# Kernel optimization log

Measured on AMD Instinct MI355X. Metric: run time of the kernel, lower is better.

Reference implementation:

```python
import jax, jax.numpy as jnp
import numpy as np

B, T, D = 16, 2048, 64


def setup_inputs() -> dict:
    key = jax.random.key(0)
    kq, kk, kv, kb = jax.random.split(key, 4)
    q = jax.random.normal(kq, (B, T, D), dtype=jnp.float32)
    k = jax.random.normal(kk, (B, T, D), dtype=jnp.float32)
    v = jax.random.normal(kv, (B, T, D), dtype=jnp.float32)
    add_attn = jax.random.normal(kb, (B, T, T), dtype=jnp.float32)
    return {"q": q, "k": k, "v": v, "add_attn": add_attn}


def reference(q, k, v, add_attn):
    # scale = 1/sqrt(head_dim), the standard value passed by callers
    scale = 1.0 / jnp.sqrt(jnp.asarray(q.shape[-1], dtype=q.dtype))
    # [B, T, T] attention logits: bmm(q, k^T) * scale + additive bias
    attn = jnp.einsum('btd,bsd->bts', q, k) * scale + add_attn
    # softmax over keys (dim=2); dropout p=0.0 is identity
    attn = jax.nn.softmax(attn, axis=2)
    # [B, T, D] weighted values
    output = jnp.einsum('bts,bsd->btd', attn, v)
    return (output, attn)
```

## Files before the change

### kernel.cpp

```cpp
#include <hip/hip_runtime.h>
#include <stdint.h>

#define NB 16
#define NT 2048
#define ND 64

typedef __attribute__((ext_vector_type(8))) short bf16x8;
typedef __attribute__((ext_vector_type(4))) float f32x4;
typedef __attribute__((ext_vector_type(4))) _Float16 f16x4;

__device__ __forceinline__ unsigned short f2bf(float f) {
    union { float f; unsigned u; } v; v.f = f;
    unsigned r = v.u + 0x7fffu + ((v.u >> 16) & 1u);
    return (unsigned short)(r >> 16);
}
__device__ __forceinline__ unsigned short f2h(float f) {
    union { _Float16 h; unsigned short u; } v; v.h = (_Float16)f; return v.u;
}

__global__ __launch_bounds__(256) void prep_k(const float* __restrict__ Q,
                                              const float* __restrict__ K,
                                              const float* __restrict__ V,
                                              unsigned short* __restrict__ qbf,
                                              unsigned short* __restrict__ kbf,
                                              unsigned short* __restrict__ vt)
{
    const size_t i = (size_t)blockIdx.x * 256 + threadIdx.x;
    const int which = blockIdx.y;
    if (which == 2) {
        float4 v4 = ((const float4*)V)[i];
        const int d4 = (int)(i & 15);
        const int t  = (int)((i >> 4) & (NT - 1));
        const int b  = (int)(i >> 15);
        unsigned short* base = vt + ((size_t)b * ND + d4 * 4) * NT + t;
        base[0]      = f2h(v4.x);
        base[NT]     = f2h(v4.y);
        base[2 * NT] = f2h(v4.z);
        base[3 * NT] = f2h(v4.w);
    } else {
        const float4* src = (which == 0) ? (const float4*)Q : (const float4*)K;
        unsigned short* dst = (which == 0) ? qbf : kbf;
        float4 v4 = src[i];
        union { unsigned short s[4]; unsigned long long ll; } u;
        u.s[0] = f2bf(v4.x); u.s[1] = f2bf(v4.y);
        u.s[2] = f2bf(v4.z); u.s[3] = f2bf(v4.w);
        *(unsigned long long*)(dst + 4 * i) = u.ll;
    }
}

__global__ __launch_bounds__(256, 2)
void attn_onepass(const unsigned short* __restrict__ qbf,
                  const unsigned short* __restrict__ kbf,
                  const unsigned short* __restrict__ vt,
                  const float* __restrict__ Bias,
                  float* __restrict__ Out,
                  float* __restrict__ Attn)
{
    const int b = blockIdx.y, q0 = blockIdx.x * 16;
    const int tid = threadIdx.x, w = tid >> 6, lane = tid & 63;
    const int n = lane & 15, qd = lane >> 4;
    const int kw0 = w * 512;

    __shared__ float s_rs[4][16];
    __shared__ float s_o[4 * 16 * 68];

    const unsigned short* qp = qbf + ((size_t)(b * NT + q0 + n)) * ND + qd * 8;
    const bf16x8 qf0 = *(const bf16x8*)qp;
    const bf16x8 qf1 = *(const bf16x8*)(qp + 32);
    const float* Bb = Bias + ((size_t)b * NT + q0 + n) * NT;
    float* Ab = Attn + ((size_t)b * NT + q0 + n) * NT;
    const unsigned short* vtb = vt + (size_t)b * ND * NT + (size_t)n * NT;

    f16x4 ev[32];
    bf16x8 kb0[6], kb1[6];
    float4 bb[8];
#pragma unroll
    for (int i = 0; i < 6; ++i) {
        const unsigned short* kp = kbf + ((size_t)(b * NT + kw0 + 16 * i + n)) * ND + qd * 8;
        kb0[i] = *(const bf16x8*)kp;
        kb1[i] = *(const bf16x8*)(kp + 32);
    }
#pragma unroll
    for (int i = 0; i < 8; ++i)
        bb[i] = *(const float4*)(Bb + kw0 + 16 * i + qd * 4);
    __builtin_amdgcn_sched_barrier(0);

    float rs = 0.f;
#pragma unroll
    for (int t = 0; t < 32; ++t) {
        const bf16x8 kf0 = kb0[t % 6];
        const bf16x8 kf1 = kb1[t % 6];
        const float4 bs = bb[t & 7];
        f32x4 acc = {0.f, 0.f, 0.f, 0.f};
        acc = __builtin_amdgcn_mfma_f32_16x16x32_bf16(kf0, qf0, acc, 0, 0, 0);
        acc = __builtin_amdgcn_mfma_f32_16x16x32_bf16(kf1, qf1, acc, 0, 0, 0);
        float e0 = __expf(__builtin_fmaf(acc[0], 0.125f, bs.x - 2.0f));
        float e1 = __expf(__builtin_fmaf(acc[1], 0.125f, bs.y - 2.0f));
        float e2 = __expf(__builtin_fmaf(acc[2], 0.125f, bs.z - 2.0f));
        float e3 = __expf(__builtin_fmaf(acc[3], 0.125f, bs.w - 2.0f));
        union { _Float16 h[4]; f16x4 v; } u;
        u.h[0] = (_Float16)e0; u.h[1] = (_Float16)e1;
        u.h[2] = (_Float16)e2; u.h[3] = (_Float16)e3;
        ev[t] = u.v;
        rs += (e0 + e1) + (e2 + e3);
        __builtin_amdgcn_sched_barrier(0);
        if (t + 6 < 32) {
            const unsigned short* kp =
                kbf + ((size_t)(b * NT + kw0 + 16 * (t + 6) + n)) * ND + qd * 8;
            kb0[t % 6] = *(const bf16x8*)kp;
            kb1[t % 6] = *(const bf16x8*)(kp + 32);
        }
        if (t + 8 < 32)
            bb[t & 7] = *(const float4*)(Bb + kw0 + 16 * (t + 8) + qd * 4);
        __builtin_amdgcn_sched_barrier(0);
    }

    f16x4 vr0[4][4], vr1[4][4];
#pragma unroll
    for (int i = 0; i < 4; ++i)
#pragma unroll
        for (int dt = 0; dt < 4; ++dt) {
            const unsigned short* vp = vtb + kw0 + 32 * i + qd * 4 + (size_t)dt * 16 * NT;
            vr0[i][dt] = *(const f16x4*)(const void*)vp;
            vr1[i][dt] = *(const f16x4*)(const void*)(vp + 16);
        }
    __builtin_amdgcn_sched_barrier(0);

    rs += __shfl_xor(rs, 16, 64);
    rs += __shfl_xor(rs, 32, 64);
    if (lane < 16) s_rs[w][lane] = rs;
    __syncthreads();
    const float tot = (s_rs[0][n] + s_rs[1][n]) + (s_rs[2][n] + s_rs[3][n]);
    const float inv = 1.0f / tot;

    f32x4 oacc[4];
#pragma unroll
    for (int dt = 0; dt < 4; ++dt) oacc[dt] = (f32x4){0.f, 0.f, 0.f, 0.f};

#pragma unroll
    for (int tp = 0; tp < 16; ++tp) {
        const int key0 = kw0 + 32 * tp;
        f16x4 va0[4], va1[4];
#pragma unroll
        for (int dt = 0; dt < 4; ++dt) { va0[dt] = vr0[tp & 3][dt]; va1[dt] = vr1[tp & 3][dt]; }
        const f16x4 e0v = ev[2 * tp];
        const f16x4 e1v = ev[2 * tp + 1];
        float4 s0, s1;
        s0.x = (float)e0v[0] * inv; s0.y = (float)e0v[1] * inv;
        s0.z = (float)e0v[2] * inv; s0.w = (float)e0v[3] * inv;
        s1.x = (float)e1v[0] * inv; s1.y = (float)e1v[1] * inv;
        s1.z = (float)e1v[2] * inv; s1.w = (float)e1v[3] * inv;
        *(float4*)(Ab + key0 + qd * 4) = s0;
        *(float4*)(Ab + key0 + 16 + qd * 4) = s1;
#pragma unroll
        for (int dt = 0; dt < 4; ++dt) {
            oacc[dt] = __builtin_amdgcn_mfma_f32_16x16x16f16(va0[dt], e0v, oacc[dt], 0, 0, 0);
            oacc[dt] = __builtin_amdgcn_mfma_f32_16x16x16f16(va1[dt], e1v, oacc[dt], 0, 0, 0);
        }
        __builtin_amdgcn_sched_barrier(0);
        if (tp + 4 < 16) {
#pragma unroll
            for (int dt = 0; dt < 4; ++dt) {
                const unsigned short* vp =
                    vtb + kw0 + 32 * (tp + 4) + qd * 4 + (size_t)dt * 16 * NT;
                vr0[tp & 3][dt] = *(const f16x4*)(const void*)vp;
                vr1[tp & 3][dt] = *(const f16x4*)(const void*)(vp + 16);
            }
        }
        __builtin_amdgcn_sched_barrier(0);
    }

#pragma unroll
    for (int dt = 0; dt < 4; ++dt) {
        float4 t4;
        t4.x = oacc[dt][0] * inv; t4.y = oacc[dt][1] * inv;
        t4.z = oacc[dt][2] * inv; t4.w = oacc[dt][3] * inv;
        *(float4*)&s_o[(w * 16 + n) * 68 + dt * 16 + qd * 4] = t4;
    }
    __syncthreads();
    {
        const int row = tid >> 4, d4 = (tid & 15) * 4;
        float4 o0 = *(const float4*)&s_o[(0 * 16 + row) * 68 + d4];
        float4 o1 = *(const float4*)&s_o[(1 * 16 + row) * 68 + d4];
        float4 o2 = *(const float4*)&s_o[(2 * 16 + row) * 68 + d4];
        float4 o3 = *(const float4*)&s_o[(3 * 16 + row) * 68 + d4];
        float4 o;
        o.x = (o0.x + o1.x) + (o2.x + o3.x);
        o.y = (o0.y + o1.y) + (o2.y + o3.y);
        o.z = (o0.z + o1.z) + (o2.z + o3.z);
        o.w = (o0.w + o1.w) + (o2.w + o3.w);
        *(float4*)(Out + ((size_t)b * NT + q0 + row) * ND + d4) = o;
    }
}

__device__ __forceinline__ bf16x8 pack8(float4 a, float4 b) {
    union { unsigned short s[8]; bf16x8 v; } u;
    u.s[0] = f2bf(a.x); u.s[1] = f2bf(a.y); u.s[2] = f2bf(a.z); u.s[3] = f2bf(a.w);
    u.s[4] = f2bf(b.x); u.s[5] = f2bf(b.y); u.s[6] = f2bf(b.z); u.s[7] = f2bf(b.w);
    return u.v;
}
__global__ __launch_bounds__(256, 2)
void attn_fused(const float* __restrict__ Q, const float* __restrict__ K,
                const float* __restrict__ V, const float* __restrict__ Bias,
                float* __restrict__ Out, float* __restrict__ Attn)
{
    const int b  = blockIdx.y;
    const int q0 = blockIdx.x * 16;
    const int tid  = threadIdx.x;
    const int w    = tid >> 6;
    const int lane = tid & 63;
    const int n  = lane & 15;
    const int qd = lane >> 4;
    const int kw0 = w * 512;
    __shared__ float s_rs[4][16];
    __shared__ __align__(16) unsigned char s_rp[4][16 * 80];
    const float* Qb = Q + ((size_t)b * NT + q0) * ND;
    const float* Kb = K + (size_t)b * NT * ND;
    const float* Vb = V + (size_t)b * NT * ND;
    const float* Bb = Bias + ((size_t)b * NT + q0) * NT;
    float* Ab = Attn + ((size_t)b * NT + q0) * NT;
    float* Ob = Out  + ((size_t)b * NT + q0) * ND;
    bf16x8 qf0, qf1;
    {
        const float* qp = Qb + n * ND + qd * 8;
        qf0 = pack8(*(const float4*)qp,        *(const float4*)(qp + 4));
        qf1 = pack8(*(const float4*)(qp + 32), *(const float4*)(qp + 36));
    }
    float ev[32][4];
    float rs = 0.f;
#pragma unroll
    for (int t = 0; t < 32; ++t) {
        const int key0 = kw0 + 16 * t;
        const float* kp = Kb + (size_t)(key0 + n) * ND + qd * 8;
        bf16x8 kf0 = pack8(*(const float4*)kp,        *(const float4*)(kp + 4));
        bf16x8 kf1 = pack8(*(const float4*)(kp + 32), *(const float4*)(kp + 36));
        f32x4 acc = {0.f, 0.f, 0.f, 0.f};
        acc = __builtin_amdgcn_mfma_f32_16x16x32_bf16(kf0, qf0, acc, 0, 0, 0);
        acc = __builtin_amdgcn_mfma_f32_16x16x32_bf16(kf1, qf1, acc, 0, 0, 0);
        float4 bs = *(const float4*)(Bb + (size_t)n * NT + key0 + qd * 4);
        float e0 = __expf(acc[0] * 0.125f + bs.x);
        float e1 = __expf(acc[1] * 0.125f + bs.y);
        float e2 = __expf(acc[2] * 0.125f + bs.z);
        float e3 = __expf(acc[3] * 0.125f + bs.w);
        ev[t][0] = e0; ev[t][1] = e1; ev[t][2] = e2; ev[t][3] = e3;
        rs += (e0 + e1) + (e2 + e3);
    }
    rs += __shfl_xor(rs, 16, 64);
    rs += __shfl_xor(rs, 32, 64);
    if (lane < 16) s_rs[w][lane] = rs;
    __syncthreads();
    const float tot = (s_rs[0][n] + s_rs[1][n]) + (s_rs[2][n] + s_rs[3][n]);
    const float inv = 1.0f / tot;
    f32x4 oacc[4];
#pragma unroll
    for (int dt = 0; dt < 4; ++dt) oacc[dt] = (f32x4){0.f, 0.f, 0.f, 0.f};
    unsigned char* rp = &s_rp[w][0];
#pragma unroll
    for (int c = 0; c < 16; ++c) {
        const int kbase = kw0 + 32 * c;
#pragma unroll
        for (int tt = 0; tt < 2; ++tt) {
            const int t = 2 * c + tt;
            float p0 = ev[t][0] * inv;
            float p1 = ev[t][1] * inv;
            float p2 = ev[t][2] * inv;
            float p3 = ev[t][3] * inv;
            float4 pv; pv.x = p0; pv.y = p1; pv.z = p2; pv.w = p3;
            *(float4*)(Ab + (size_t)n * NT + kbase + 16 * tt + qd * 4) = pv;
            union { unsigned short s[4]; unsigned long long ll; } pu;
            pu.s[0] = f2bf(p0); pu.s[1] = f2bf(p1);
            pu.s[2] = f2bf(p2); pu.s[3] = f2bf(p3);
            *(unsigned long long*)(rp + n * 80 + (16 * tt + 4 * qd) * 2) = pu.ll;
        }
        __syncthreads();
        bf16x8 pf;
        {
            union { uint4 u; bf16x8 v; } uu;
            uu.u = *(const uint4*)(rp + n * 80 + qd * 16);
            pf = uu.v;
        }
#pragma unroll
        for (int dt = 0; dt < 4; ++dt) {
            const int d = dt * 16 + n;
            const float* vp = Vb + (size_t)(kbase + qd * 8) * ND + d;
            float4 va, vb4;
            va.x  = vp[0];   va.y  = vp[64];  va.z  = vp[128]; va.w  = vp[192];
            vb4.x = vp[256]; vb4.y = vp[320]; vb4.z = vp[384]; vb4.w = vp[448];
            bf16x8 vf = pack8(va, vb4);
            oacc[dt] = __builtin_amdgcn_mfma_f32_16x16x32_bf16(vf, pf, oacc[dt], 0, 0, 0);
        }
        __syncthreads();
    }
#pragma unroll
    for (int dt = 0; dt < 4; ++dt)
#pragma unroll
        for (int r = 0; r < 4; ++r)
            atomicAdd(Ob + (size_t)n * ND + dt * 16 + qd * 4 + r, oacc[dt][r]);
}

extern "C" void kernel_launch(void* const* d_in, const int* in_sizes, int n_in,
                              void* d_out, int out_size, void* d_ws, size_t ws_size,
                              hipStream_t stream)
{
    const float* q    = (const float*)d_in[0];
    const float* k    = (const float*)d_in[1];
    const float* v    = (const float*)d_in[2];
    const float* bias = (const float*)d_in[3];
    float* out  = (float*)d_out;
    float* attn = out + (size_t)NB * NT * ND;

    const size_t elems = (size_t)NB * NT * ND;
    const size_t need  = 3 * elems * 2;

    if (ws_size >= need) {
        unsigned short* qbf = (unsigned short*)d_ws;
        unsigned short* kbf = qbf + elems;
        unsigned short* vtb = kbf + elems;
        prep_k<<<dim3((unsigned)(elems / 4 / 256), 3), 256, 0, stream>>>(q, k, v, qbf, kbf, vtb);
        attn_onepass<<<dim3(NT / 16, NB), 256, 0, stream>>>(qbf, kbf, vtb, bias, out, attn);
    } else {
        hipMemsetAsync(out, 0, (size_t)NB * NT * ND * sizeof(float), stream);
        dim3 grid(NT / 16, NB);
        attn_fused<<<grid, 256, 0, stream>>>(q, k, v, bias, out, attn);
    }
}
```

Measured before the change: 242.6 us.

## Burst-prefetch bias into triple buffers and remap block order across batches

Replaces the per-iteration sliding prefetch of bias and K with bursts of eight bias loads into three rotating register buffers, keeping up to 24 tiles in flight. The K prefetch distance drops from six to four to save registers. Block indices are also remapped so consecutively launched blocks are spread across batches. The aim is to hide bias-stream latency behind the MFMA and exp work, at the cost of higher register pressure and different cache locality for K and V.

```diff
diff --git a/kernel.cpp b/kernel.cpp
--- a/kernel.cpp
+++ b/kernel.cpp
@@ -48,6 +48,37 @@
     }
 }
 
+#define LOAD_BURST(BUF, T0)                                              \
+  _Pragma("unroll")                                                      \
+  for (int j = 0; j < 8; ++j)                                            \
+    BUF[j] = *(const f32x4*)(bbp + 16 * ((T0) + j));
+
+#define PH1_GROUP(BUF, TB)                                                   \
+  _Pragma("unroll")                                                          \
+  for (int j = 0; j < 8; ++j) {                                              \
+    const int t = (TB) * 8 + j;                                              \
+    const bf16x8 kf0 = kb0[t & 3];                                           \
+    const bf16x8 kf1 = kb1[t & 3];                                           \
+    const f32x4 bs = BUF[j];                                                 \
+    f32x4 acc = {0.f, 0.f, 0.f, 0.f};                                        \
+    acc = __builtin_amdgcn_mfma_f32_16x16x32_bf16(kf0, qf0, acc, 0, 0, 0);   \
+    acc = __builtin_amdgcn_mfma_f32_16x16x32_bf16(kf1, qf1, acc, 0, 0, 0);   \
+    float e0 = __expf(__builtin_fmaf(acc[0], 0.125f, bs[0] - 2.0f));         \
+    float e1 = __expf(__builtin_fmaf(acc[1], 0.125f, bs[1] - 2.0f));         \
+    float e2 = __expf(__builtin_fmaf(acc[2], 0.125f, bs[2] - 2.0f));         \
+    float e3 = __expf(__builtin_fmaf(acc[3], 0.125f, bs[3] - 2.0f));         \
+    union { _Float16 h[4]; f16x4 v; } u;                                     \
+    u.h[0] = (_Float16)e0; u.h[1] = (_Float16)e1;                            \
+    u.h[2] = (_Float16)e2; u.h[3] = (_Float16)e3;                            \
+    ev[t] = u.v;                                                             \
+    rs += (e0 + e1) + (e2 + e3);                                             \
+    if (t + 4 < 32) {                                                        \
+      const unsigned short* kp = kbp + (size_t)(16 * (t + 4)) * ND;          \
+      kb0[t & 3] = *(const bf16x8*)kp;                                       \
+      kb1[t & 3] = *(const bf16x8*)(kp + 32);                                \
+    }                                                                        \
+  }
+
 __global__ __launch_bounds__(256, 2)
 void attn_onepass(const unsigned short* __restrict__ qbf,
                   const unsigned short* __restrict__ kbf,
@@ -56,7 +87,11 @@
                   float* __restrict__ Out,
                   float* __restrict__ Attn)
 {
-    const int b = blockIdx.y, q0 = blockIdx.x * 16;
+    const int flat = blockIdx.x + (NT / 16) * blockIdx.y;
+    const int lin  = (flat & 7) * 256 + (flat >> 3);
+    const int b    = lin >> 7;
+    const int q0   = (lin & 127) * 16;
+
     const int tid = threadIdx.x, w = tid >> 6, lane = tid & 63;
     const int n = lane & 15, qd = lane >> 4;
     const int kw0 = w * 512;
@@ -70,50 +105,36 @@
     const float* Bb = Bias + ((size_t)b * NT + q0 + n) * NT;
     float* Ab = Attn + ((size_t)b * NT + q0 + n) * NT;
     const unsigned short* vtb = vt + (size_t)b * ND * NT + (size_t)n * NT;
+    const unsigned short* kbp = kbf + ((size_t)(b * NT + kw0 + n)) * ND + qd * 8;
+    const float* bbp = Bb + kw0 + qd * 4;
 
     f16x4 ev[32];
-    bf16x8 kb0[6], kb1[6];
-    float4 bb[8];
-#pragma unroll
-    for (int i = 0; i < 6; ++i) {
-        const unsigned short* kp = kbf + ((size_t)(b * NT + kw0 + 16 * i + n)) * ND + qd * 8;
+    bf16x8 kb0[4], kb1[4];
+    f32x4 bbA[8], bbB[8], bbC[8];
+
+#pragma unroll
+    for (int i = 0; i < 4; ++i) {
+        const unsigned short* kp = kbp + (size_t)(16 * i) * ND;
         kb0[i] = *(const bf16x8*)kp;
         kb1[i] = *(const bf16x8*)(kp + 32);
     }
-#pragma unroll
-    for (int i = 0; i < 8; ++i)
-        bb[i] = *(const float4*)(Bb + kw0 + 16 * i + qd * 4);
+    LOAD_BURST(bbA, 0)
+    __builtin_amdgcn_sched_barrier(0);
+    LOAD_BURST(bbB, 8)
+    __builtin_amdgcn_sched_barrier(0);
+    LOAD_BURST(bbC, 16)
     __builtin_amdgcn_sched_barrier(0);
 
     float rs = 0.f;
-#pragma unroll
-    for (int t = 0; t < 32; ++t) {
-        const bf16x8 kf0 = kb0[t % 6];
-        const bf16x8 kf1 = kb1[t % 6];
-        const float4 bs = bb[t & 7];
-        f32x4 acc = {0.f, 0.f, 0.f, 0.f};
-        acc = __builtin_amdgcn_mfma_f32_16x16x32_bf16(kf0, qf0, acc, 0, 0, 0);
-        acc = __builtin_amdgcn_mfma_f32_16x16x32_bf16(kf1, qf1, acc, 0, 0, 0);
-        float e0 = __expf(__builtin_fmaf(acc[0], 0.125f, bs.x - 2.0f));
-        float e1 = __expf(__builtin_fmaf(acc[1], 0.125f, bs.y - 2.0f));
-        float e2 = __expf(__builtin_fmaf(acc[2], 0.125f, bs.z - 2.0f));
-        float e3 = __expf(__builtin_fmaf(acc[3], 0.125f, bs.w - 2.0f));
-        union { _Float16 h[4]; f16x4 v; } u;
-        u.h[0] = (_Float16)e0; u.h[1] = (_Float16)e1;
-        u.h[2] = (_Float16)e2; u.h[3] = (_Float16)e3;
-        ev[t] = u.v;
-        rs += (e0 + e1) + (e2 + e3);
-        __builtin_amdgcn_sched_barrier(0);
-        if (t + 6 < 32) {
-            const unsigned short* kp =
-                kbf + ((size_t)(b * NT + kw0 + 16 * (t + 6) + n)) * ND + qd * 8;
-            kb0[t % 6] = *(const bf16x8*)kp;
-            kb1[t % 6] = *(const bf16x8*)(kp + 32);
-        }
-        if (t + 8 < 32)
-            bb[t & 7] = *(const float4*)(Bb + kw0 + 16 * (t + 8) + qd * 4);
-        __builtin_amdgcn_sched_barrier(0);
-    }
+    PH1_GROUP(bbA, 0)
+    __builtin_amdgcn_sched_barrier(0);
+    LOAD_BURST(bbA, 24)
+    __builtin_amdgcn_sched_barrier(0);
+    PH1_GROUP(bbB, 1)
+    __builtin_amdgcn_sched_barrier(0);
+    PH1_GROUP(bbC, 2)
+    __builtin_amdgcn_sched_barrier(0);
+    PH1_GROUP(bbA, 3)
 
     f16x4 vr0[4][4], vr1[4][4];
 #pragma unroll
```

Measured after the change: 243.4 us, median of 2. About the same (+0.4%).
